# Performance work log

Measured on AMD Instinct MI355X. Metric: run time of the kernel, lower is better.

## Reference

```python
import jax, jax.numpy as jnp
import numpy as np

LATENT = 256
SELEN = 64
MSIZE = 8
BS = 32
T = 2048
TOUCH_IN = 3
GAZE_IN = 4


def setup_inputs() -> dict:
    key = jax.random.key(0)
    ks = jax.random.split(key, 16)
    kH = 1.0 / np.sqrt(LATENT)

    def u(k, shape):
        return jax.random.uniform(k, shape, jnp.float32, -kH, kH)

    return {
        "touch_d": jax.random.normal(ks[0], (BS, T, TOUCH_IN), jnp.float32),
        "gaze_d": jax.random.normal(ks[1], (BS, T, GAZE_IN), jnp.float32),
        # scale so start + SELEN <= T always (avoids the random fallback branch)
        "l": jax.random.uniform(ks[2], (BS, MSIZE), jnp.float32) * ((T - SELEN) / T),
        "tW_ih": u(ks[3], (4 * LATENT, TOUCH_IN)),
        "tW_hh": u(ks[4], (4 * LATENT, LATENT)),
        "tb_ih": u(ks[5], (4 * LATENT,)),
        "tb_hh": u(ks[6], (4 * LATENT,)),
        "gW_ih": u(ks[7], (4 * LATENT, GAZE_IN)),
        "gW_hh": u(ks[8], (4 * LATENT, LATENT)),
        "gb_ih": u(ks[9], (4 * LATENT,)),
        "gb_hh": u(ks[10], (4 * LATENT,)),
        "t_lin_w": u(ks[11], (LATENT, LATENT)),
        "t_lin_b": u(ks[12], (LATENT,)),
        "g_lin_w": u(ks[13], (LATENT, LATENT)),
        "g_lin_b": u(ks[14], (LATENT,)),
    }


def lstm(x, W_ih, W_hh, b_ih, b_hh):
    # x: [B, T, D] -> outputs [B, T, H]; PyTorch gate order i, f, g, o
    B = x.shape[0]
    H = W_hh.shape[1]
    x_proj = x @ W_ih.T + (b_ih + b_hh)  # [B, T, 4H] precomputed input GEMM

    def step(carry, xt):
        h, c = carry
        gates = xt + h @ W_hh.T
        i, f, g, o = jnp.split(gates, 4, axis=-1)
        c = jax.nn.sigmoid(f) * c + jax.nn.sigmoid(i) * jnp.tanh(g)
        h = jax.nn.sigmoid(o) * jnp.tanh(c)
        return (h, c), h

    h0 = jnp.zeros((B, H), x.dtype)
    _, ys = jax.lax.scan(step, (h0, h0), jnp.swapaxes(x_proj, 0, 1))
    return jnp.swapaxes(ys, 0, 1)


def glimpse_mean(emb, starts):
    # emb: [B, T, H]; starts: [B, M] int window starts; mean over M windows of SELEN
    idx = (starts[:, :, None] + jnp.arange(SELEN)).reshape(emb.shape[0], MSIZE * SELEN)
    gathered = jnp.take_along_axis(emb, idx[..., None], axis=1)  # [B, M*SELEN, H]
    return gathered.mean(axis=1)


def reference(touch_d, gaze_d, l, tW_ih, tW_hh, tb_ih, tb_hh,
              gW_ih, gW_hh, gb_ih, gb_hh, t_lin_w, t_lin_b, g_lin_w, g_lin_b):
    touch_out = lstm(touch_d, tW_ih, tW_hh, tb_ih, tb_hh)
    gaze_out = lstm(gaze_d, gW_ih, gW_hh, gb_ih, gb_hh)
    touch_emb = jax.nn.relu(touch_out) @ t_lin_w.T + t_lin_b  # [B, T, H]
    gaze_emb = jax.nn.relu(gaze_out) @ g_lin_w.T + g_lin_b

    touch_mean = touch_emb.mean(axis=1)
    gaze_mean = gaze_emb.mean(axis=1)

    starts = (l * T).astype(jnp.int32)  # [B, M], guaranteed start + SELEN <= T
    touch_attn = glimpse_mean(touch_emb, starts)
    gaze_attn = glimpse_mean(gaze_emb, starts)

    return jnp.concatenate([touch_mean, touch_attn, gaze_mean, gaze_attn], axis=-1)
```

## Files before the change

### kernel.cpp

```cpp
#include <hip/hip_runtime.h>

#define HDIM 256
#define TLEN 2048
#define SELEN 64
#define MSZ 8

typedef _Float16 f16x2 __attribute__((ext_vector_type(2)));
typedef unsigned int u32x16 __attribute__((ext_vector_type(16)));

__device__ __forceinline__ float dot2f(unsigned int w, unsigned int h, float acc) {
  return __builtin_amdgcn_fdot2(__builtin_bit_cast(f16x2, w),
                                __builtin_bit_cast(f16x2, h), acc, false);
}

__device__ __forceinline__ unsigned int pack2(float a, float b) {
  f16x2 v;
  v.x = (_Float16)a; v.y = (_Float16)b;
  return __builtin_bit_cast(unsigned int, v);
}

__device__ __forceinline__ float sigm(float x)   { return 1.0f / (1.0f + __expf(-x)); }
__device__ __forceinline__ float tanh_f(float x) { return 1.0f - 2.0f / (__expf(2.0f * x) + 1.0f); }

#define WO_OFF    0
#define WIH_OFF   131072
#define CNT_OFF   147456
#define H2_OFF    149504
#define LDS_BYTES 150528

__shared__ __align__(16) unsigned char smem[LDS_BYTES];

#define LOADG16(V, RP, B) do {                                                  \
    float2 a0 = (RP)[(B)+0],  a1 = (RP)[(B)+1],  a2 = (RP)[(B)+2],  a3 = (RP)[(B)+3];   \
    float2 a4 = (RP)[(B)+4],  a5 = (RP)[(B)+5],  a6 = (RP)[(B)+6],  a7 = (RP)[(B)+7];   \
    float2 a8 = (RP)[(B)+8],  a9 = (RP)[(B)+9],  aA = (RP)[(B)+10], aB = (RP)[(B)+11];  \
    float2 aC = (RP)[(B)+12], aD = (RP)[(B)+13], aE = (RP)[(B)+14], aF = (RP)[(B)+15];  \
    V[0]  = pack2(a0.x, a0.y); V[1]  = pack2(a1.x, a1.y);                       \
    V[2]  = pack2(a2.x, a2.y); V[3]  = pack2(a3.x, a3.y);                       \
    V[4]  = pack2(a4.x, a4.y); V[5]  = pack2(a5.x, a5.y);                       \
    V[6]  = pack2(a6.x, a6.y); V[7]  = pack2(a7.x, a7.y);                       \
    V[8]  = pack2(a8.x, a8.y); V[9]  = pack2(a9.x, a9.y);                       \
    V[10] = pack2(aA.x, aA.y); V[11] = pack2(aB.x, aB.y);                       \
    V[12] = pack2(aC.x, aC.y); V[13] = pack2(aD.x, aD.y);                       \
    V[14] = pack2(aE.x, aE.y); V[15] = pack2(aF.x, aF.y);                       \
    __builtin_amdgcn_sched_barrier(0);                                          \
  } while (0)

#define JBLK(WIv, WFv, WGv, Q, HC, OC, PF, JN)                                  \
  { const uint4 hh = HC, wo = OC;                                               \
    if (PF) { HC = hv4[JN]; OC = wo4r[(JN) * 512]; }                            \
    ai = dot2f(WIv[4*(Q)+0], hh.x, ai); af = dot2f(WFv[4*(Q)+0], hh.x, af);     \
    ag = dot2f(WGv[4*(Q)+0], hh.x, ag); ao = dot2f(wo.x,         hh.x, ao);     \
    ai = dot2f(WIv[4*(Q)+1], hh.y, ai); af = dot2f(WFv[4*(Q)+1], hh.y, af);     \
    ag = dot2f(WGv[4*(Q)+1], hh.y, ag); ao = dot2f(wo.y,         hh.y, ao);     \
    ai = dot2f(WIv[4*(Q)+2], hh.z, ai); af = dot2f(WFv[4*(Q)+2], hh.z, af);     \
    ag = dot2f(WGv[4*(Q)+2], hh.z, ag); ao = dot2f(wo.z,         hh.z, ao);     \
    ai = dot2f(WIv[4*(Q)+3], hh.w, ai); af = dot2f(WFv[4*(Q)+3], hh.w, af);     \
    ag = dot2f(WGv[4*(Q)+3], hh.w, ag); ao = dot2f(wo.w,         hh.w, ao);     \
    __builtin_amdgcn_sched_barrier(0); }

__global__ void
__attribute__((amdgpu_flat_work_group_size(512, 512), amdgpu_waves_per_eu(2, 2)))
lstm_seq_kernel(const float* __restrict__ touch, const float* __restrict__ gaze,
                const float* __restrict__ l,
                const float* __restrict__ tWih, const float* __restrict__ tWhh,
                const float* __restrict__ tbih, const float* __restrict__ tbhh,
                const float* __restrict__ gWih, const float* __restrict__ gWhh,
                const float* __restrict__ gbih, const float* __restrict__ gbhh,
                float* __restrict__ ws)
{
  const int bid  = (int)blockIdx.x;
  const int lsel = bid >> 5;
  const int b    = bid & 31;
  const int tid  = (int)threadIdx.x;
  const int lane = tid & 63;
  const int wv   = tid >> 6;
  const int n    = wv * 32 + (lane & 31);
  const int kh   = lane >> 5;
  const int c0   = kh * 128;

  const float* __restrict__ x   = lsel ? gaze : touch;
  const float* __restrict__ Wih = lsel ? gWih : tWih;
  const float* __restrict__ Whh = lsel ? gWhh : tWhh;
  const float* __restrict__ bih = lsel ? gbih : tbih;
  const float* __restrict__ bhh = lsel ? gbhh : tbhh;
  const int D = lsel ? 4 : 3;

  unsigned int*  woL  = (unsigned int*)(smem + WO_OFF);
  float4*        wihF = (float4*)(smem + WIH_OFF);
  unsigned char* cntL = smem + CNT_OFF;

  u32x16 wi0, wi1, wi2, wi3, wf0, wf1, wf2, wf3, wg0, wg1, wg2, wg3;
  {
    const float2* ri = (const float2*)(Whh + (size_t)n * HDIM + c0);
    const float2* rf = (const float2*)(Whh + (size_t)(n + 256) * HDIM + c0);
    const float2* rg = (const float2*)(Whh + (size_t)(n + 512) * HDIM + c0);
    LOADG16(wi0, ri, 0);  LOADG16(wi1, ri, 16);  LOADG16(wi2, ri, 32);  LOADG16(wi3, ri, 48);
    LOADG16(wf0, rf, 0);  LOADG16(wf1, rf, 16);  LOADG16(wf2, rf, 32);  LOADG16(wf3, rf, 48);
    LOADG16(wg0, rg, 0);  LOADG16(wg1, rg, 16);  LOADG16(wg2, rg, 32);  LOADG16(wg3, rg, 48);
  }
  {
    const float2* ro = (const float2*)(Whh + (size_t)(n + 768) * HDIM + c0);
    uint4* wo4 = (uint4*)woL;
    #pragma unroll
    for (int jb = 0; jb < 4; ++jb) {
      #pragma unroll
      for (int q = 0; q < 4; ++q) {
        const int j = jb * 4 + q;
        float2 e0 = ro[4*j], e1 = ro[4*j+1], e2 = ro[4*j+2], e3 = ro[4*j+3];
        uint4 v;
        v.x = pack2(e0.x, e0.y); v.y = pack2(e1.x, e1.y);
        v.z = pack2(e2.x, e2.y); v.w = pack2(e3.x, e3.y);
        wo4[j * 512 + tid] = v;
      }
      __builtin_amdgcn_sched_barrier(0);
    }
  }

  for (int r = tid; r < 1024; r += 512) {
    const float* wr = Wih + (size_t)r * D;
    float4 v;
    v.x = wr[0]; v.y = wr[1]; v.z = wr[2];
    v.w = (D == 4) ? wr[3] : 0.0f;
    wihF[r] = v;
  }
  __builtin_amdgcn_sched_barrier(0);

  {
    int s0 = (int)(l[b * MSZ + 0] * 2048.0f), s1 = (int)(l[b * MSZ + 1] * 2048.0f);
    int s2 = (int)(l[b * MSZ + 2] * 2048.0f), s3 = (int)(l[b * MSZ + 3] * 2048.0f);
    int s4 = (int)(l[b * MSZ + 4] * 2048.0f), s5 = (int)(l[b * MSZ + 5] * 2048.0f);
    int s6 = (int)(l[b * MSZ + 6] * 2048.0f), s7 = (int)(l[b * MSZ + 7] * 2048.0f);
    for (int t0 = tid; t0 < TLEN; t0 += 512) {
      int c = 0;
      c += (t0 >= s0 && t0 < s0 + SELEN) ? 1 : 0;
      c += (t0 >= s1 && t0 < s1 + SELEN) ? 1 : 0;
      c += (t0 >= s2 && t0 < s2 + SELEN) ? 1 : 0;
      c += (t0 >= s3 && t0 < s3 + SELEN) ? 1 : 0;
      c += (t0 >= s4 && t0 < s4 + SELEN) ? 1 : 0;
      c += (t0 >= s5 && t0 < s5 + SELEN) ? 1 : 0;
      c += (t0 >= s6 && t0 < s6 + SELEN) ? 1 : 0;
      c += (t0 >= s7 && t0 < s7 + SELEN) ? 1 : 0;
      cntL[t0] = (unsigned char)c;
    }
  }

  if (tid < 128) ((unsigned int*)(smem + H2_OFF))[tid] = 0u;

  const float bi_ = bih[n]       + bhh[n];
  const float bf_ = bih[n + 256] + bhh[n + 256];
  const float bg_ = bih[n + 512] + bhh[n + 512];
  const float bo_ = bih[n + 768] + bhh[n + 768];

  float cst = 0.f, Sall = 0.f, Swin = 0.f;
  const float* xrow = x + (size_t)b * TLEN * D;

  float x0 = xrow[0], x1 = xrow[1], x2 = xrow[2];
  float x3 = (D == 4) ? xrow[3] : 0.0f;

  __syncthreads();

  float cw = (float)cntL[0];
  const uint4* wo4r = ((const uint4*)woL) + tid;

  for (int t = 0; t < TLEN; ++t) {
    const int tn = (t + 1 < TLEN) ? (t + 1) : t;
    const float* xp = xrow + (size_t)tn * D;
    const float nx0 = xp[0], nx1 = xp[1], nx2 = xp[2];
    const float nx3 = (D == 4) ? xp[3] : 0.0f;
    const float ncw = (float)cntL[tn];

    const uint4* hv4 = (const uint4*)(smem + H2_OFF + (t & 1) * 512 + kh * 256);

    uint4 hA = hv4[0], oA = wo4r[0];
    uint4 hB = hv4[1], oB = wo4r[512];

    float ai = 0.f, af = 0.f, ag = 0.f, ao = 0.f;
    JBLK(wi0, wf0, wg0, 0, hA, oA, 1,  2)
    JBLK(wi0, wf0, wg0, 1, hB, oB, 1,  3)
    JBLK(wi0, wf0, wg0, 2, hA, oA, 1,  4)
    JBLK(wi0, wf0, wg0, 3, hB, oB, 1,  5)
    JBLK(wi1, wf1, wg1, 0, hA, oA, 1,  6)
    JBLK(wi1, wf1, wg1, 1, hB, oB, 1,  7)
    JBLK(wi1, wf1, wg1, 2, hA, oA, 1,  8)
    JBLK(wi1, wf1, wg1, 3, hB, oB, 1,  9)
    JBLK(wi2, wf2, wg2, 0, hA, oA, 1, 10)
    JBLK(wi2, wf2, wg2, 1, hB, oB, 1, 11)
    JBLK(wi2, wf2, wg2, 2, hA, oA, 1, 12)
    JBLK(wi2, wf2, wg2, 3, hB, oB, 1, 13)
    JBLK(wi3, wf3, wg3, 0, hA, oA, 1, 14)
    JBLK(wi3, wf3, wg3, 1, hB, oB, 1, 15)
    JBLK(wi3, wf3, wg3, 2, hA, oA, 0,  0)
    JBLK(wi3, wf3, wg3, 3, hB, oB, 0,  0)

    ai += __shfl_xor(ai, 32);
    af += __shfl_xor(af, 32);
    ag += __shfl_xor(ag, 32);
    ao += __shfl_xor(ao, 32);

    const float4 wr0 = wihF[n];
    const float4 wr1 = wihF[n + 256];
    const float4 wr2 = wihF[n + 512];
    const float4 wr3 = wihF[n + 768];
    const float gi = ai + bi_ + x0*wr0.x + x1*wr0.y + x2*wr0.z + x3*wr0.w;
    const float gf = af + bf_ + x0*wr1.x + x1*wr1.y + x2*wr1.z + x3*wr1.w;
    const float gg = ag + bg_ + x0*wr2.x + x1*wr2.y + x2*wr2.z + x3*wr2.w;
    const float go = ao + bo_ + x0*wr3.x + x1*wr3.y + x2*wr3.z + x3*wr3.w;
    const float si = sigm(gi), sf = sigm(gf), so = sigm(go);
    const float tg = tanh_f(gg);
    cst = sf * cst + si * tg;
    const float hv = so * tanh_f(cst);
    const float rh = fmaxf(hv, 0.0f);
    Sall += rh;
    Swin += cw * rh;

    if (kh == 0)
      ((_Float16*)(smem + H2_OFF + ((t + 1) & 1) * 512))[n] = (_Float16)hv;

    x0 = nx0; x1 = nx1; x2 = nx2; x3 = nx3; cw = ncw;

    __syncthreads();
  }

  if (kh == 0) {
    ws[((0 * 2 + lsel) * 32 + b) * HDIM + n] = Sall;
    ws[((1 * 2 + lsel) * 32 + b) * HDIM + n] = Swin;
  }
}

__global__ void proj_kernel(const float* __restrict__ ws,
                            const float* __restrict__ tlw, const float* __restrict__ tlb,
                            const float* __restrict__ glw, const float* __restrict__ glb,
                            float* __restrict__ out)
{
  const int b    = (int)blockIdx.x >> 2;
  const int seg  = (int)blockIdx.x & 3;
  const int j    = (int)threadIdx.x;
  const int lsel = seg >> 1;
  const int kind = seg & 1;
  const float* __restrict__ W    = lsel ? glw : tlw;
  const float* __restrict__ bias = lsel ? glb : tlb;
  const float scale = kind ? (1.0f / 512.0f) : (1.0f / 2048.0f);

  __shared__ float Sv[HDIM];
  Sv[j] = ws[((kind * 2 + lsel) * 32 + b) * HDIM + j] * scale;
  __syncthreads();

  float acc = bias[j];
  const float4* wr4 = (const float4*)(W + (size_t)j * HDIM);
  #pragma unroll 8
  for (int k4 = 0; k4 < HDIM / 4; ++k4) {
    const float4 w = wr4[k4];
    acc = fmaf(Sv[4*k4],     w.x, acc);
    acc = fmaf(Sv[4*k4 + 1], w.y, acc);
    acc = fmaf(Sv[4*k4 + 2], w.z, acc);
    acc = fmaf(Sv[4*k4 + 3], w.w, acc);
  }
  out[(size_t)b * 1024 + seg * HDIM + j] = acc;
}

extern "C" void kernel_launch(void* const* d_in, const int* in_sizes, int n_in,
                              void* d_out, int out_size, void* d_ws, size_t ws_size,
                              hipStream_t stream) {
  (void)in_sizes; (void)n_in; (void)out_size; (void)ws_size;
  const float* touch = (const float*)d_in[0];
  const float* gaze  = (const float*)d_in[1];
  const float* l     = (const float*)d_in[2];
  const float* tWih  = (const float*)d_in[3];
  const float* tWhh  = (const float*)d_in[4];
  const float* tbih  = (const float*)d_in[5];
  const float* tbhh  = (const float*)d_in[6];
  const float* gWih  = (const float*)d_in[7];
  const float* gWhh  = (const float*)d_in[8];
  const float* gbih  = (const float*)d_in[9];
  const float* gbhh  = (const float*)d_in[10];
  const float* tlw   = (const float*)d_in[11];
  const float* tlb   = (const float*)d_in[12];
  const float* glw   = (const float*)d_in[13];
  const float* glb   = (const float*)d_in[14];
  float* out = (float*)d_out;
  float* ws  = (float*)d_ws;

  hipLaunchKernelGGL(lstm_seq_kernel, dim3(64), dim3(512), 0, stream,
                     touch, gaze, l, tWih, tWhh, tbih, tbhh,
                     gWih, gWhh, gbih, gbhh, ws);
  hipLaunchKernelGGL(proj_kernel, dim3(128), dim3(256), 0, stream,
                     ws, tlw, tlb, glw, glb, out);
}
```

Baseline: 3.469 ms.

## Stream forget/cell gate weights from global memory instead of registers

Forget and cell-gate recurrent weights move out of registers into a packed fp16 workspace, filled by a new pre-kernel and reloaded from global memory (L2) on every timestep. The register-pinned waves_per_eu hint is dropped, and the per-step input x is no longer prefetched but read each step through readfirstlane as a uniform value. The aim is to cut register pressure, at the cost of roughly doubling per-step memory traffic on the serial critical path, where that traffic has latency.

```diff
diff --git a/kernel.cpp b/kernel.cpp
--- a/kernel.cpp
+++ b/kernel.cpp
@@ -17,6 +17,10 @@
   f16x2 v;
   v.x = (_Float16)a; v.y = (_Float16)b;
   return __builtin_bit_cast(unsigned int, v);
+}
+
+__device__ __forceinline__ float uni(float v) {
+  return __builtin_bit_cast(float, __builtin_amdgcn_readfirstlane(__builtin_bit_cast(int, v)));
 }
 
 __device__ __forceinline__ float sigm(float x)   { return 1.0f / (1.0f + __expf(-x)); }
@@ -29,6 +33,9 @@
 #define LDS_BYTES 150528
 
 __shared__ __align__(16) unsigned char smem[LDS_BYTES];
+
+#define WS_FG_U4   16384
+#define WS_OUT_F   131072
 
 #define LOADG16(V, RP, B) do {                                                  \
     float2 a0 = (RP)[(B)+0],  a1 = (RP)[(B)+1],  a2 = (RP)[(B)+2],  a3 = (RP)[(B)+3];   \
@@ -46,21 +53,46 @@
     __builtin_amdgcn_sched_barrier(0);                                          \
   } while (0)
 
-#define JBLK(WIv, WFv, WGv, Q, HC, OC, PF, JN)                                  \
-  { const uint4 hh = HC, wo = OC;                                               \
-    if (PF) { HC = hv4[JN]; OC = wo4r[(JN) * 512]; }                            \
-    ai = dot2f(WIv[4*(Q)+0], hh.x, ai); af = dot2f(WFv[4*(Q)+0], hh.x, af);     \
-    ag = dot2f(WGv[4*(Q)+0], hh.x, ag); ao = dot2f(wo.x,         hh.x, ao);     \
-    ai = dot2f(WIv[4*(Q)+1], hh.y, ai); af = dot2f(WFv[4*(Q)+1], hh.y, af);     \
-    ag = dot2f(WGv[4*(Q)+1], hh.y, ag); ao = dot2f(wo.y,         hh.y, ao);     \
-    ai = dot2f(WIv[4*(Q)+2], hh.z, ai); af = dot2f(WFv[4*(Q)+2], hh.z, af);     \
-    ag = dot2f(WGv[4*(Q)+2], hh.z, ag); ao = dot2f(wo.z,         hh.z, ao);     \
-    ai = dot2f(WIv[4*(Q)+3], hh.w, ai); af = dot2f(WFv[4*(Q)+3], hh.w, af);     \
-    ag = dot2f(WGv[4*(Q)+3], hh.w, ag); ao = dot2f(wo.w,         hh.w, ao);     \
+#define JBLK(WIv, Q, HC, OC, FC, GC, PF, JN)                                    \
+  { const uint4 hh = HC, wo = OC, wf = FC, wg = GC;                             \
+    if (PF) { HC = hv4[JN]; OC = wo4r[(JN) * 512];                              \
+              FC = fgS[(JN) * 512]; GC = fgS[(16 + (JN)) * 512]; }              \
+    ai = dot2f(WIv[4*(Q)+0], hh.x, ai); af = dot2f(wf.x, hh.x, af);             \
+    ag = dot2f(wg.x,         hh.x, ag); ao = dot2f(wo.x, hh.x, ao);             \
+    ai = dot2f(WIv[4*(Q)+1], hh.y, ai); af = dot2f(wf.y, hh.y, af);             \
+    ag = dot2f(wg.y,         hh.y, ag); ao = dot2f(wo.y, hh.y, ao);             \
+    ai = dot2f(WIv[4*(Q)+2], hh.z, ai); af = dot2f(wf.z, hh.z, af);             \
+    ag = dot2f(wg.z,         hh.z, ag); ao = dot2f(wo.z, hh.z, ao);             \
+    ai = dot2f(WIv[4*(Q)+3], hh.w, ai); af = dot2f(wf.w, hh.w, af);             \
+    ag = dot2f(wg.w,         hh.w, ag); ao = dot2f(wo.w, hh.w, ao);             \
     __builtin_amdgcn_sched_barrier(0); }
 
+__global__ __launch_bounds__(512)
+void pack_fg_kernel(const float* __restrict__ tWhh, const float* __restrict__ gWhh,
+                    float* __restrict__ ws)
+{
+  const int bid  = (int)blockIdx.x;
+  const int lsel = bid >> 5;
+  const int j    = bid & 31;
+  const int tid  = (int)threadIdx.x;
+  const int lane = tid & 63;
+  const int wv   = tid >> 6;
+  const int n    = wv * 32 + (lane & 31);
+  const int kh   = lane >> 5;
+  const int c0   = kh * 128;
+
+  const float* __restrict__ Whh = lsel ? gWhh : tWhh;
+  const int row = ((j < 16) ? 256 : 512) + n;
+  const int k0  = c0 + 8 * (j & 15);
+  const float* p = Whh + (size_t)row * HDIM + k0;
+  uint4 v;
+  v.x = pack2(p[0], p[1]); v.y = pack2(p[2], p[3]);
+  v.z = pack2(p[4], p[5]); v.w = pack2(p[6], p[7]);
+  ((uint4*)ws)[lsel * WS_FG_U4 + j * 512 + tid] = v;
+}
+
 __global__ void
-__attribute__((amdgpu_flat_work_group_size(512, 512), amdgpu_waves_per_eu(2, 2)))
+__attribute__((amdgpu_flat_work_group_size(512, 512)))
 lstm_seq_kernel(const float* __restrict__ touch, const float* __restrict__ gaze,
                 const float* __restrict__ l,
                 const float* __restrict__ tWih, const float* __restrict__ tWhh,
@@ -90,14 +122,11 @@
   float4*        wihF = (float4*)(smem + WIH_OFF);
   unsigned char* cntL = smem + CNT_OFF;
 
-  u32x16 wi0, wi1, wi2, wi3, wf0, wf1, wf2, wf3, wg0, wg1, wg2, wg3;
+  u32x16 wi0, wi1, wi2, wi3;
   {
     const float2* ri = (const float2*)(Whh + (size_t)n * HDIM + c0);
-    const float2* rf = (const float2*)(Whh + (size_t)(n + 256) * HDIM + c0);
-    const float2* rg = (const float2*)(Whh + (size_t)(n + 512) * HDIM + c0);
-    LOADG16(wi0, ri, 0);  LOADG16(wi1, ri, 16);  LOADG16(wi2, ri, 32);  LOADG16(wi3, ri, 48);
-    LOADG16(wf0, rf, 0);  LOADG16(wf1, rf, 16);  LOADG16(wf2, rf, 32);  LOADG16(wf3, rf, 48);
-    LOADG16(wg0, rg, 0);  LOADG16(wg1, rg, 16);  LOADG16(wg2, rg, 32);  LOADG16(wg3, rg, 48);
+    LOADG16(wi0, ri, 0);  LOADG16(wi1, ri, 16);
+    LOADG16(wi2, ri, 32); LOADG16(wi3, ri, 48);
   }
   {
     const float2* ro = (const float2*)(Whh + (size_t)(n + 768) * HDIM + c0);
@@ -155,43 +184,39 @@
   float cst = 0.f, Sall = 0.f, Swin = 0.f;
   const float* xrow = x + (size_t)b * TLEN * D;
 
-  float x0 = xrow[0], x1 = xrow[1], x2 = xrow[2];
-  float x3 = (D == 4) ? xrow[3] : 0.0f;
-
   __syncthreads();
 
-  float cw = (float)cntL[0];
   const uint4* wo4r = ((const uint4*)woL) + tid;
+  const uint4* fgS  = ((const uint4*)ws) + lsel * WS_FG_U4 + tid;
 
   for (int t = 0; t < TLEN; ++t) {
-    const int tn = (t + 1 < TLEN) ? (t + 1) : t;
-    const float* xp = xrow + (size_t)tn * D;
-    const float nx0 = xp[0], nx1 = xp[1], nx2 = xp[2];
-    const float nx3 = (D == 4) ? xp[3] : 0.0f;
-    const float ncw = (float)cntL[tn];
+    const float* xp = xrow + (size_t)t * D;
+    const float x0 = uni(xp[0]), x1 = uni(xp[1]), x2 = uni(xp[2]);
+    const float x3 = (D == 4) ? uni(xp[3]) : 0.0f;
+    const float cw = (float)cntL[t];
 
     const uint4* hv4 = (const uint4*)(smem + H2_OFF + (t & 1) * 512 + kh * 256);
 
-    uint4 hA = hv4[0], oA = wo4r[0];
-    uint4 hB = hv4[1], oB = wo4r[512];
+    uint4 hA = hv4[0], oA = wo4r[0],   fA = fgS[0],       gA = fgS[16 * 512];
+    uint4 hB = hv4[1], oB = wo4r[512], fB = fgS[512],     gB = fgS[17 * 512];
 
     float ai = 0.f, af = 0.f, ag = 0.f, ao = 0.f;
-    JBLK(wi0, wf0, wg0, 0, hA, oA, 1,  2)
-    JBLK(wi0, wf0, wg0, 1, hB, oB, 1,  3)
-    JBLK(wi0, wf0, wg0, 2, hA, oA, 1,  4)
-    JBLK(wi0, wf0, wg0, 3, hB, oB, 1,  5)
-    JBLK(wi1, wf1, wg1, 0, hA, oA, 1,  6)
-    JBLK(wi1, wf1, wg1, 1, hB, oB, 1,  7)
-    JBLK(wi1, wf1, wg1, 2, hA, oA, 1,  8)
-    JBLK(wi1, wf1, wg1, 3, hB, oB, 1,  9)
-    JBLK(wi2, wf2, wg2, 0, hA, oA, 1, 10)
-    JBLK(wi2, wf2, wg2, 1, hB, oB, 1, 11)
-    JBLK(wi2, wf2, wg2, 2, hA, oA, 1, 12)
-    JBLK(wi2, wf2, wg2, 3, hB, oB, 1, 13)
-    JBLK(wi3, wf3, wg3, 0, hA, oA, 1, 14)
-    JBLK(wi3, wf3, wg3, 1, hB, oB, 1, 15)
-    JBLK(wi3, wf3, wg3, 2, hA, oA, 0,  0)
-    JBLK(wi3, wf3, wg3, 3, hB, oB, 0,  0)
+    JBLK(wi0, 0, hA, oA, fA, gA, 1,  2)
+    JBLK(wi0, 1, hB, oB, fB, gB, 1,  3)
+    JBLK(wi0, 2, hA, oA, fA, gA, 1,  4)
+    JBLK(wi0, 3, hB, oB, fB, gB, 1,  5)
+    JBLK(wi1, 0, hA, oA, fA, gA, 1,  6)
+    JBLK(wi1, 1, hB, oB, fB, gB, 1,  7)
+    JBLK(wi1, 2, hA, oA, fA, gA, 1,  8)
+    JBLK(wi1, 3, hB, oB, fB, gB, 1,  9)
+    JBLK(wi2, 0, hA, oA, fA, gA, 1, 10)
+    JBLK(wi2, 1, hB, oB, fB, gB, 1, 11)
+    JBLK(wi2, 2, hA, oA, fA, gA, 1, 12)
+    JBLK(wi2, 3, hB, oB, fB, gB, 1, 13)
+    JBLK(wi3, 0, hA, oA, fA, gA, 1, 14)
+    JBLK(wi3, 1, hB, oB, fB, gB, 1, 15)
+    JBLK(wi3, 2, hA, oA, fA, gA, 0,  0)
+    JBLK(wi3, 3, hB, oB, fB, gB, 0,  0)
 
     ai += __shfl_xor(ai, 32);
     af += __shfl_xor(af, 32);
@@ -217,14 +242,12 @@
     if (kh == 0)
       ((_Float16*)(smem + H2_OFF + ((t + 1) & 1) * 512))[n] = (_Float16)hv;
 
-    x0 = nx0; x1 = nx1; x2 = nx2; x3 = nx3; cw = ncw;
-
     __syncthreads();
   }
 
   if (kh == 0) {
-    ws[((0 * 2 + lsel) * 32 + b) * HDIM + n] = Sall;
-    ws[((1 * 2 + lsel) * 32 + b) * HDIM + n] = Swin;
+    ws[WS_OUT_F + ((0 * 2 + lsel) * 32 + b) * HDIM + n] = Sall;
+    ws[WS_OUT_F + ((1 * 2 + lsel) * 32 + b) * HDIM + n] = Swin;
   }
 }
 
@@ -243,7 +266,7 @@
   const float scale = kind ? (1.0f / 512.0f) : (1.0f / 2048.0f);
 
   __shared__ float Sv[HDIM];
-  Sv[j] = ws[((kind * 2 + lsel) * 32 + b) * HDIM + j] * scale;
+  Sv[j] = ws[WS_OUT_F + ((kind * 2 + lsel) * 32 + b) * HDIM + j] * scale;
   __syncthreads();
 
   float acc = bias[j];
@@ -281,6 +304,8 @@
   float* out = (float*)d_out;
   float* ws  = (float*)d_ws;
 
+  hipLaunchKernelGGL(pack_fg_kernel, dim3(64), dim3(512), 0, stream,
+                     tWhh, gWhh, ws);
   hipLaunchKernelGGL(lstm_seq_kernel, dim3(64), dim3(512), 0, stream,
                      touch, gaze, l, tWih, tWhh, tbih, tbhh,
                      gWih, gWhh, gbih, gbhh, ws);
```

After: 4.788 ms. +38.0%, slower.
